# Optimization experiments

Measured on AMD Instinct MI355X. Metric: run time of the kernel, lower is better.

## Reference

```python
import jax, jax.numpy as jnp
import numpy as np

WIDE = 15
PAD = (WIDE - 1) // 2
FREQS = np.array([1., 2., 3., 4., 5., 6.], dtype=np.float32)  # wave_base_ml frequencies


def _lstm_dir(x, wih, whh, b):
    # x: [B,T,F]; wih: [4H,F]; whh: [4H,H]; b: [4H] (b_ih+b_hh fused)
    H = whh.shape[1]
    xg = jnp.einsum('btf,gf->btg', x, wih) + b  # precompute input projections
    def step(carry, xt):
        h, c = carry
        g = xt + h @ whh.T
        i, f, gg, o = jnp.split(g, 4, axis=-1)  # torch gate order i,f,g,o
        c = jax.nn.sigmoid(f) * c + jax.nn.sigmoid(i) * jnp.tanh(gg)
        h = jax.nn.sigmoid(o) * jnp.tanh(c)
        return (h, c), h
    h0 = jnp.zeros((x.shape[0], H), x.dtype)
    _, hs = jax.lax.scan(step, (h0, h0), jnp.swapaxes(xg, 0, 1))
    return jnp.swapaxes(hs, 0, 1)


def _bn(x, g, b, eps=1e-5):
    # training-mode BatchNorm1d over (N, L) per channel; x: [B,C,L]
    m = jnp.mean(x, axis=(0, 2), keepdims=True)
    v = jnp.var(x, axis=(0, 2), keepdims=True)
    return (x - m) * jax.lax.rsqrt(v + eps) * g[None, :, None] + b[None, :, None]


def _conv1d(x, w, b):
    y = jax.lax.conv_general_dilated(x, w, (1,), 'VALID', dimension_numbers=('NCH', 'OIH', 'NCH'))
    return y + b[None, :, None]


def _haar(x):
    s = 0.7071067811865476
    return (x[..., ::2] + x[..., 1::2]) * s, (x[..., ::2] - x[..., 1::2]) * s


def _forward(x, lstm_wif, lstm_whf, lstm_bf, lstm_wir, lstm_whr, lstm_br, base_w, base_b,
             g1, be1, g2, be2, g3, be3, g4, be4, g5, be5,
             w2, b2, w3, b3, w4, b4, w5, b5, fcw, fcb):
    xt = jnp.swapaxes(x, 1, 2)  # [B,T,F]
    fwd = _lstm_dir(xt, lstm_wif, lstm_whf, lstm_bf)
    bwd = _lstm_dir(xt[:, ::-1], lstm_wir, lstm_whr, lstm_br)[:, ::-1]
    X = jnp.swapaxes(jnp.concatenate([fwd, bwd], axis=-1), 1, 2)  # [B,C,T], C=2*dim
    B, C, T = X.shape
    Xp = jnp.pad(X, ((0, 0), (0, 0), (PAD, PAD)))
    # shared sliding windows [B,C,T,WIDE] used both for scale conv and Furi_conv
    Xwin = jnp.stack([Xp[..., k:k + T] for k in range(WIDE)], axis=-1)
    offs = (jnp.arange(WIDE, dtype=X.dtype) - PAD) / WIDE
    outs = []
    for ii in range(len(FREQS)):
        scales = jax.nn.relu(jnp.einsum('bctk,k->bct', Xwin, base_w[ii]) + base_b[ii])
        # per-position cosine Fourier basis generated from the learned scales
        bases = jnp.cos((2.0 * np.pi * FREQS[ii]) * scales[..., None] * offs)  # [B,C,T,WIDE]
        o = jnp.sum(Xwin * bases, axis=-1)  # position-dependent (dynamic) conv
        sqrs = jnp.sqrt((jnp.trunc(scales * WIDE) + 1.0) / (WIDE + 2) * 2.0)
        outs.append(o / sqrs)
    wave = jnp.stack(outs, axis=1).reshape(B, -1, T)  # [B, n_waves*C, T] (wave-major, matches torch cat+view)
    out = _bn(wave, g1, be1)
    out = _bn(jax.nn.relu(_conv1d(out, w2, b2)), g2, be2)
    out = _bn(jax.nn.relu(_conv1d(out, w3, b3)), g3, be3)
    out_back = out  # [B, V_dim, L3]
    out = _bn(jax.nn.relu(_conv1d(out, w4, b4)), g4, be4)  # [B,16,L3-2]
    # 4-level Haar DWT; 5 subbands upsampled to L3, averaged over channels
    a1, d1 = _haar(out_back); a2, d2 = _haar(a1); a3, d3 = _haar(a2); a4, d4 = _haar(a3)
    L3 = out_back.shape[-1]
    bands = [jnp.repeat(bb, L3 // bb.shape[-1], axis=-1) for bb in (a4, d4, d3, d2, d1)]
    dwt = jnp.stack([bb.mean(axis=1) for bb in bands], axis=1)  # [B,5,L3]
    odwt = _bn(jax.nn.relu(_conv1d(dwt, w5, b5)), g5, be5)  # [B,16,L3-2]
    out = jnp.concatenate([out, odwt], axis=-1)
    out = out.mean(axis=-1)  # AdaptiveAvgPool1d(1) + squeeze
    return out @ fcw.T + fcb


def setup_inputs() -> dict:
    key = jax.random.key(0)
    ks = iter(jax.random.split(key, 40))
    def p(shape, s=0.05):
        return jax.random.normal(next(ks), shape, jnp.float32) * s
    B, F, T, DIM, NW, Vd = 32, 64, 518, 64, 6, 32
    C = 2 * DIM
    return {
        'x': jax.random.normal(next(ks), (B, F, T), jnp.float32),
        'lstm_wif': p((4 * DIM, F)), 'lstm_whf': p((4 * DIM, DIM)), 'lstm_bf': p((4 * DIM,)),
        'lstm_wir': p((4 * DIM, F)), 'lstm_whr': p((4 * DIM, DIM)), 'lstm_br': p((4 * DIM,)),
        'base_w': p((NW, WIDE)), 'base_b': p((NW,)),
        'g1': jnp.ones((C * NW,)), 'be1': jnp.zeros((C * NW,)),
        'g2': jnp.ones((128,)), 'be2': jnp.zeros((128,)),
        'g3': jnp.ones((Vd,)), 'be3': jnp.zeros((Vd,)),
        'g4': jnp.ones((16,)), 'be4': jnp.zeros((16,)),
        'g5': jnp.ones((16,)), 'be5': jnp.zeros((16,)),
        'w2': p((128, C * NW, 3)), 'b2': p((128,)),
        'w3': p((Vd, 128, 5)), 'b3': p((Vd,)),
        'w4': p((16, Vd, 3)), 'b4': p((16,)),
        'w5': p((16, 5, 3)), 'b5': p((16,)),
        'fcw': p((10, 16)), 'fcb': p((10,)),
    }


def reference(x, lstm_wif, lstm_whf, lstm_bf, lstm_wir, lstm_whr, lstm_br, base_w, base_b,
              g1, be1, g2, be2, g3, be3, g4, be4, g5, be5,
              w2, b2, w3, b3, w4, b4, w5, b5, fcw, fcb):
    return _forward(x, lstm_wif, lstm_whf, lstm_bf, lstm_wir, lstm_whr, lstm_br, base_w, base_b,
                    g1, be1, g2, be2, g3, be3, g4, be4, g5, be5,
                    w2, b2, w3, b3, w4, b4, w5, b5, fcw, fcb)
```

## Files before the change

### kernel.cpp

```cpp
#include <hip/hip_runtime.h>
#include <math.h>

#define B_     32
#define F_     64
#define T_     518
#define HID    64
#define GATES  256
#define CCH    128
#define NWAVE  6
#define WCH    768
#define L2_    516
#define L3_    512
#define L4_    510

__device__ __forceinline__ float frcp(float x) { return __builtin_amdgcn_rcpf(x); }
__device__ __forceinline__ float fsigmoid(float x) { return frcp(1.f + __expf(-x)); }
__device__ __forceinline__ float ftanh(float x) { return 1.f - 2.f * frcp(1.f + __expf(2.f * x)); }

__global__ void xg_kernel(const float* __restrict__ x,
                          const float* __restrict__ wif, const float* __restrict__ bf,
                          const float* __restrict__ wir, const float* __restrict__ br,
                          float* __restrict__ xg_f, float* __restrict__ xg_r,
                          float* __restrict__ stats) {
    if (blockIdx.x == 0 && blockIdx.y == 0) {
        for (int i = threadIdx.x; i < 2 * WCH; i += 256) stats[i] = 0.f;
    }
    const int tid = threadIdx.x;
    const int wv  = tid >> 7;
    const int g2  = tid & 1;
    const int r   = (tid >> 1) & 63;
    const int g   = (2 * wv + g2) * 64 + r;
    const int b   = blockIdx.y;
    const int t0  = blockIdx.x * 8;
    float4 wa[16], wb[16];
    const float4* w0 = (const float4*)(wif + g * F_);
    const float4* w1 = (const float4*)(wir + g * F_);
#pragma unroll
    for (int i = 0; i < 16; ++i) { wa[i] = w0[i]; wb[i] = w1[i]; }
    const float bfv = bf[g], brv = br[g];
    for (int tt = 0; tt < 8; ++tt) {
        const int t = t0 + tt;
        if (t >= T_) break;
        const float* xp = x + (size_t)b * F_ * T_ + t;
        float a0 = bfv, a1 = brv;
#pragma unroll
        for (int i = 0; i < 16; ++i) {
            float x0 = xp[(i * 4 + 0) * T_];
            float x1 = xp[(i * 4 + 1) * T_];
            float x2 = xp[(i * 4 + 2) * T_];
            float x3 = xp[(i * 4 + 3) * T_];
            a0 += wa[i].x * x0 + wa[i].y * x1 + wa[i].z * x2 + wa[i].w * x3;
            a1 += wb[i].x * x0 + wb[i].y * x1 + wb[i].z * x2 + wb[i].w * x3;
        }
        const size_t o = ((size_t)b * T_ + t) * GATES + tid;
        xg_f[o] = a0;
        xg_r[o] = a1;
    }
}

__global__ __launch_bounds__(128, 1) void lstm_kernel(
        const float* __restrict__ xgi_f, const float* __restrict__ xgi_r,
        const float* __restrict__ whf, const float* __restrict__ whr,
        float* __restrict__ X) {
    const int dir = blockIdx.x & 1;
    const int b   = blockIdx.x >> 1;
    const float* xg  = (dir ? xgi_r : xgi_f) + (size_t)b * T_ * GATES;
    const float* whh = dir ? whr : whf;
    const int tid = threadIdx.x;
    const int r   = tid & 63;
    const int w   = tid >> 6;

    float4 wA[16], wB[16];
    {
        const float4* pA = (const float4*)(whh + (size_t)((2 * w) * HID + r) * HID);
        const float4* pB = (const float4*)(whh + (size_t)((2 * w + 1) * HID + r) * HID);
#pragma unroll
        for (int i = 0; i < 16; ++i) { wA[i] = pA[i]; wB[i] = pB[i]; }
    }

    __shared__ __align__(16) float hs[2][HID];
    __shared__ __align__(16) float gbuf[2][HID][4];
    hs[w][r] = 0.f;
    float c = 0.f;
    float* Xrow = X + ((size_t)(b * CCH + dir * HID + r)) * T_;

    int t = dir ? (T_ - 1) : 0;
    const int step = dir ? -1 : 1;
    const float2* xg2 = (const float2*)xg;
    float2 q0 = xg2[((size_t)t * 2 + w) * 64 + r];
    float2 q1 = xg2[((size_t)(t + step) * 2 + w) * 64 + r];

    for (int s = 0; s < T_; ++s) {
        float4 a0 = {q0.x, 0.f, 0.f, 0.f};
        float4 a1 = {q0.y, 0.f, 0.f, 0.f};
        const float4* h4p = (const float4*)hs[w];
#pragma unroll
        for (int i = 0; i < 16; ++i) {
            const float4 h4 = h4p[i];
            a0.x = fmaf(wA[i].x, h4.x, a0.x); a0.y = fmaf(wA[i].y, h4.y, a0.y);
            a0.z = fmaf(wA[i].z, h4.z, a0.z); a0.w = fmaf(wA[i].w, h4.w, a0.w);
            a1.x = fmaf(wB[i].x, h4.x, a1.x); a1.y = fmaf(wB[i].y, h4.y, a1.y);
            a1.z = fmaf(wB[i].z, h4.z, a1.z); a1.w = fmaf(wB[i].w, h4.w, a1.w);
        }
        const float gA = (a0.x + a0.y) + (a0.z + a0.w);
        const float gB = (a1.x + a1.y) + (a1.z + a1.w);
        const int buf = s & 1;
        *(float2*)&gbuf[buf][r][2 * w] = make_float2(gA, gB);

        int tp = t + 2 * step;
        tp = tp < 0 ? 0 : (tp >= T_ ? T_ - 1 : tp);
        const float2 qn = xg2[((size_t)tp * 2 + w) * 64 + r];

        asm volatile("s_waitcnt lgkmcnt(0)" ::: "memory");
        __builtin_amdgcn_s_barrier();

        const float4 g4 = *(const float4*)gbuf[buf][r];
        const float si = fsigmoid(g4.x);
        const float sf = fsigmoid(g4.y);
        const float so = fsigmoid(g4.w);
        c = sf * c + si * ftanh(g4.z);
        const float h = so * ftanh(c);

        hs[w][r] = h;
        if (w == 0) Xrow[t] = h;
        q0 = q1; q1 = qn;
        t += step;
    }
}

__global__ void wave_kernel(const float* __restrict__ X,
                            const float* __restrict__ bw, const float* __restrict__ bb,
                            float* __restrict__ wave, float* __restrict__ stats) {
    const int b = blockIdx.z, c = blockIdx.y;
    const int t0 = blockIdx.x * 256;
    const int tid = threadIdx.x;
    __shared__ float xs[256 + 14];
    __shared__ float bws[NWAVE][16];
    __shared__ float bbs[NWAVE];
    __shared__ float red[4][12];
    const float* xrow = X + ((size_t)(b * CCH + c)) * T_;
    for (int i = tid; i < 270; i += 256) {
        int tt = t0 - 7 + i;
        xs[i] = (tt >= 0 && tt < T_) ? xrow[tt] : 0.f;
    }
    if (tid < NWAVE * 15) bws[tid / 15][tid % 15] = bw[tid];
    if (tid < NWAVE) bbs[tid] = bb[tid];
    __syncthreads();
    const int t = t0 + tid;
    float ls[NWAVE], lq[NWAVE];
#pragma unroll
    for (int ii = 0; ii < NWAVE; ++ii) { ls[ii] = 0.f; lq[ii] = 0.f; }
    if (t < T_) {
        float win[15];
#pragma unroll
        for (int k = 0; k < 15; ++k) win[k] = xs[tid + k];
        float e[8];
        e[0] = win[7];
#pragma unroll
        for (int m = 1; m < 8; ++m) e[m] = win[7 - m] + win[7 + m];
        const float c0 = 6.28318530717958647692f / 15.f;
#pragma unroll
        for (int ii = 0; ii < NWAVE; ++ii) {
            float sc = bbs[ii];
#pragma unroll
            for (int k = 0; k < 15; ++k) sc += win[k] * bws[ii][k];
            sc = fmaxf(sc, 0.f);
            const float phi = c0 * (float)(ii + 1) * sc;
            float o = e[0];
#pragma unroll
            for (int m = 1; m < 8; ++m) o += e[m] * __cosf(phi * (float)m);
            const float q = (truncf(sc * 15.f) + 1.f) * (2.f / 17.f);
            const float val = o * rsqrtf(q);
            wave[((size_t)(b * WCH + ii * CCH + c)) * T_ + t] = val;
            ls[ii] = val;
            lq[ii] = val * val;
        }
    }
#pragma unroll
    for (int off = 32; off > 0; off >>= 1) {
#pragma unroll
        for (int ii = 0; ii < NWAVE; ++ii) {
            ls[ii] += __shfl_down(ls[ii], off);
            lq[ii] += __shfl_down(lq[ii], off);
        }
    }
    if ((tid & 63) == 0) {
        const int w = tid >> 6;
#pragma unroll
        for (int ii = 0; ii < NWAVE; ++ii) { red[w][ii] = ls[ii]; red[w][6 + ii] = lq[ii]; }
    }
    __syncthreads();
    if (tid < 12) {
        const float a = red[0][tid] + red[1][tid] + red[2][tid] + red[3][tid];
        const int ii = tid % 6;
        const int ch = ii * CCH + c;
        atomicAdd(&stats[(tid >= 6 ? WCH : 0) + ch], a);
    }
}

__global__ void bn1_finalize_kernel(const float* __restrict__ stats,
                                    float* __restrict__ mean, float* __restrict__ rstd) {
    const int c = threadIdx.x;
    const float n = (float)(B_ * T_);
    const float m = stats[c] / n;
    const float v = stats[WCH + c] / n - m * m;
    mean[c] = m;
    rstd[c] = rsqrtf(v + 1e-5f);
}

__global__ void bn_stats_kernel(const float* __restrict__ x, int Bn, int C, int L,
                                float* __restrict__ mean, float* __restrict__ rstd) {
    const int c = blockIdx.x;
    const int tid = threadIdx.x;
    float s = 0.f, s2 = 0.f;
    for (int b = 0; b < Bn; ++b) {
        const float* row = x + ((size_t)b * C + c) * L;
        for (int l = tid; l < L; l += 256) { float v = row[l]; s += v; s2 += v * v; }
    }
#pragma unroll
    for (int off = 32; off > 0; off >>= 1) { s += __shfl_down(s, off); s2 += __shfl_down(s2, off); }
    __shared__ float ss[4], ss2[4];
    if ((tid & 63) == 0) { ss[tid >> 6] = s; ss2[tid >> 6] = s2; }
    __syncthreads();
    if (tid == 0) {
        float S = ss[0] + ss[1] + ss[2] + ss[3];
        float S2 = ss2[0] + ss2[1] + ss2[2] + ss2[3];
        float n = (float)(Bn * L);
        float m = S / n;
        float v = S2 / n - m * m;
        mean[c] = m;
        rstd[c] = rsqrtf(v + 1e-5f);
    }
}

__global__ void bnfold2_kernel(const float* __restrict__ w2, const float* __restrict__ b2,
                               const float* __restrict__ m1, const float* __restrict__ r1,
                               const float* __restrict__ g1, const float* __restrict__ be1,
                               float* __restrict__ w2t, float* __restrict__ b2t) {
    const int o = blockIdx.x, tid = threadIdx.x;
    float part = 0.f;
    for (int idx = tid; idx < WCH * 3; idx += 256) {
        const int c = idx / 3;
        const float sc = r1[c] * g1[c];
        const float sh = be1[c] - m1[c] * sc;
        const float wv = w2[(size_t)o * (WCH * 3) + idx];
        w2t[(size_t)idx * 128 + o] = wv * sc;
        part += wv * sh;
    }
#pragma unroll
    for (int off = 32; off > 0; off >>= 1) part += __shfl_down(part, off);
    __shared__ float red[4];
    if ((tid & 63) == 0) red[tid >> 6] = part;
    __syncthreads();
    if (tid == 0) b2t[o] = b2[o] + red[0] + red[1] + red[2] + red[3];
}

__global__ void bnfold3_kernel(const float* __restrict__ w3, const float* __restrict__ b3,
                               const float* __restrict__ m2, const float* __restrict__ r2,
                               const float* __restrict__ g2, const float* __restrict__ be2,
                               float* __restrict__ w3t, float* __restrict__ b3t) {
    const int o = blockIdx.x, tid = threadIdx.x;
    float part = 0.f;
    for (int idx = tid; idx < 128 * 5; idx += 256) {
        const int c = idx / 5;
        const float sc = r2[c] * g2[c];
        const float sh = be2[c] - m2[c] * sc;
        const float wv = w3[(size_t)o * 640 + idx];
        w3t[(size_t)idx * 32 + o] = wv * sc;
        part += wv * sh;
    }
#pragma unroll
    for (int off = 32; off > 0; off >>= 1) part += __shfl_down(part, off);
    __shared__ float red[4];
    if ((tid & 63) == 0) red[tid >> 6] = part;
    __syncthreads();
    if (tid == 0) b3t[o] = b3[o] + red[0] + red[1] + red[2] + red[3];
}

__global__ void bnfold4_kernel(const float* __restrict__ w4, const float* __restrict__ b4,
                               const float* __restrict__ m3, const float* __restrict__ r3,
                               const float* __restrict__ g3, const float* __restrict__ be3,
                               float* __restrict__ w4t, float* __restrict__ b4t,
                               float* __restrict__ bnp3) {
    const int o = blockIdx.x, tid = threadIdx.x;
    float part = 0.f;
    if (tid < 96) {
        const int c = tid / 3;
        const float sc = r3[c] * g3[c];
        const float sh = be3[c] - m3[c] * sc;
        const float wv = w4[(size_t)o * 96 + tid];
        w4t[(size_t)tid * 16 + o] = wv * sc;
        part = wv * sh;
    }
    if (o == 0 && tid >= 96) {
        const int ch = tid - 96;
        const float sc = r3[ch] * g3[ch];
        bnp3[ch] = sc;
        bnp3[32 + ch] = be3[ch] - m3[ch] * sc;
    }
#pragma unroll
    for (int off = 32; off > 0; off >>= 1) part += __shfl_down(part, off);
    __shared__ float red[2];
    if ((tid & 63) == 0) red[tid >> 6] = part;
    __syncthreads();
    if (tid == 0) b4t[o] = b4[o] + red[0] + red[1];
}

__global__ __launch_bounds__(256) void conv2_kernel(
        const float* __restrict__ in, const float* __restrict__ wt,
        const float* __restrict__ bt, float* __restrict__ out) {
    const int b  = blockIdx.x;
    const int t  = blockIdx.y * 256 + threadIdx.x;
    const int o0 = blockIdx.z * 16;
    if (t >= L2_) return;
    float acc[16];
#pragma unroll
    for (int j = 0; j < 16; ++j) acc[j] = bt[o0 + j];
    const float* inb = in + (size_t)b * WCH * T_ + t;
    for (int c = 0; c < WCH; ++c) {
        const float x0 = inb[c * T_], x1 = inb[c * T_ + 1], x2 = inb[c * T_ + 2];
        const float* wc = wt + (size_t)c * 384 + o0;
#pragma unroll
        for (int j = 0; j < 16; ++j)
            acc[j] = fmaf(x0, wc[j], fmaf(x1, wc[128 + j], fmaf(x2, wc[256 + j], acc[j])));
    }
    const size_t ob = ((size_t)b * 128 + o0) * L2_ + t;
#pragma unroll
    for (int j = 0; j < 16; ++j) out[ob + (size_t)j * L2_] = fmaxf(acc[j], 0.f);
}

__global__ __launch_bounds__(256) void conv3_kernel(
        const float* __restrict__ in, const float* __restrict__ wt,
        const float* __restrict__ bt, float* __restrict__ out) {
    const int b  = blockIdx.x;
    const int t  = blockIdx.y * 256 + threadIdx.x;
    const int o0 = blockIdx.z * 8;
    float acc[8];
#pragma unroll
    for (int j = 0; j < 8; ++j) acc[j] = bt[o0 + j];
    const float* inb = in + (size_t)b * 128 * L2_ + t;
    for (int c = 0; c < 128; ++c) {
        const float x0 = inb[c * L2_], x1 = inb[c * L2_ + 1], x2 = inb[c * L2_ + 2];
        const float x3 = inb[c * L2_ + 3], x4 = inb[c * L2_ + 4];
        const float* wc = wt + (size_t)c * 160 + o0;
#pragma unroll
        for (int j = 0; j < 8; ++j) {
            float a = fmaf(x0, wc[j], acc[j]);
            a = fmaf(x1, wc[32 + j], a);
            a = fmaf(x2, wc[64 + j], a);
            a = fmaf(x3, wc[96 + j], a);
            acc[j] = fmaf(x4, wc[128 + j], a);
        }
    }
    const size_t ob = ((size_t)b * 32 + o0) * L3_ + t;
#pragma unroll
    for (int j = 0; j < 8; ++j) out[ob + (size_t)j * L3_] = fmaxf(acc[j], 0.f);
}

__global__ __launch_bounds__(256) void conv4_kernel(
        const float* __restrict__ in, const float* __restrict__ wt,
        const float* __restrict__ bt, float* __restrict__ out) {
    const int b = blockIdx.x;
    const int t = blockIdx.y * 256 + threadIdx.x;
    if (t >= L4_) return;
    float acc[16];
#pragma unroll
    for (int j = 0; j < 16; ++j) acc[j] = bt[j];
    const float* inb = in + (size_t)b * 32 * L3_ + t;
    for (int c = 0; c < 32; ++c) {
        const float x0 = inb[c * L3_], x1 = inb[c * L3_ + 1], x2 = inb[c * L3_ + 2];
        const float* wc = wt + (size_t)c * 48;
#pragma unroll
        for (int j = 0; j < 16; ++j)
            acc[j] = fmaf(x0, wc[j], fmaf(x1, wc[16 + j], fmaf(x2, wc[32 + j], acc[j])));
    }
    const size_t ob = ((size_t)b * 16) * L4_ + t;
#pragma unroll
    for (int j = 0; j < 16; ++j) out[ob + (size_t)j * L4_] = fmaxf(acc[j], 0.f);
}

__global__ __launch_bounds__(512) void dwt_conv5_kernel(const float* __restrict__ y3,
                                                        const float* __restrict__ w5,
                                                        const float* __restrict__ b5,
                                                        const float* __restrict__ bnp3,
                                                        float* __restrict__ y5) {
    const int b = blockIdx.x, l = threadIdx.x;
    __shared__ float cm[L3_];
    __shared__ float bands[5][L3_];
    __shared__ float w5s[240];
    __shared__ float b5s[16];
    __shared__ float sc3s[32], sh3s[32];
    if (l < 240) w5s[l] = w5[l];
    if (l < 16) b5s[l] = b5[l];
    if (l >= 256 && l < 288) sc3s[l - 256] = bnp3[l - 256];
    if (l >= 288 && l < 320) sh3s[l - 288] = bnp3[32 + (l - 288)];
    __syncthreads();
    float s = 0.f, shs = 0.f;
    for (int ch = 0; ch < 32; ++ch) {
        s = fmaf(y3[((size_t)b * 32 + ch) * L3_ + l], sc3s[ch], s);
        shs += sh3s[ch];
    }
    cm[l] = (s + shs) * (1.f / 32.f);
    __syncthreads();
    const float s1 = 0.70710678118654752440f;
    const float s2c = 0.5f;
    const float s3 = 0.35355339059327378f;
    const float s4 = 0.25f;
    const int b16 = l & ~15, b8 = l & ~7, b4v = l & ~3, b2v = l & ~1;
    float sa = 0.f, sb = 0.f;
#pragma unroll
    for (int i = 0; i < 8; ++i) { sa += cm[b16 + i]; sb += cm[b16 + 8 + i]; }
    bands[0][l] = (sa + sb) * s4;
    bands[1][l] = (sa - sb) * s4;
    float ta = 0.f, tb = 0.f;
#pragma unroll
    for (int i = 0; i < 4; ++i) { ta += cm[b8 + i]; tb += cm[b8 + 4 + i]; }
    bands[2][l] = (ta - tb) * s3;
    bands[3][l] = (cm[b4v] + cm[b4v + 1] - cm[b4v + 2] - cm[b4v + 3]) * s2c;
    bands[4][l] = (cm[b2v] - cm[b2v + 1]) * s1;
    __syncthreads();
    if (l < L4_) {
        float in3[5][3];
#pragma unroll
        for (int c = 0; c < 5; ++c) {
            in3[c][0] = bands[c][l]; in3[c][1] = bands[c][l + 1]; in3[c][2] = bands[c][l + 2];
        }
#pragma unroll
        for (int o = 0; o < 16; ++o) {
            float acc = b5s[o];
#pragma unroll
            for (int c = 0; c < 5; ++c) {
                const float* wp = &w5s[(o * 5 + c) * 3];
                acc += in3[c][0] * wp[0] + in3[c][1] * wp[1] + in3[c][2] * wp[2];
            }
            y5[((size_t)b * 16 + o) * L4_ + l] = fmaxf(acc, 0.f);
        }
    }
}

__global__ __launch_bounds__(512) void tail_final_kernel(
        const float* __restrict__ y4, const float* __restrict__ y5,
        const float* __restrict__ g4, const float* __restrict__ be4,
        const float* __restrict__ g5, const float* __restrict__ be5,
        const float* __restrict__ fcw, const float* __restrict__ fcb,
        float* __restrict__ out) {
    const int p = threadIdx.x;
    const int b = p >> 4, ch = p & 15;
    const float2* p4 = (const float2*)(y4 + ((size_t)(b * 16 + ch)) * L4_);
    const float2* p5 = (const float2*)(y5 + ((size_t)(b * 16 + ch)) * L4_);
    float s4 = 0.f, q4 = 0.f, s5 = 0.f, q5 = 0.f;
    for (int i = 0; i < L4_ / 2; ++i) {
        float2 a = p4[i], bb2 = p5[i];
        s4 += a.x + a.y;  q4 += a.x * a.x + a.y * a.y;
        s5 += bb2.x + bb2.y; q5 += bb2.x * bb2.x + bb2.y * bb2.y;
    }
    __shared__ float S4[512], Q4[512], S5[512], Q5[512];
    __shared__ float M4[16], R4[16], M5[16], R5[16];
    __shared__ float pool[B_][16];
    S4[p] = s4; Q4[p] = q4; S5[p] = s5; Q5[p] = q5;
    __syncthreads();
    if (p < 16) {
        float ts = 0.f, tq = 0.f, us = 0.f, uq = 0.f;
        for (int bb = 0; bb < B_; ++bb) {
            ts += S4[bb * 16 + p]; tq += Q4[bb * 16 + p];
            us += S5[bb * 16 + p]; uq += Q5[bb * 16 + p];
        }
        const float n = (float)(B_ * L4_);
        float m = ts / n; M4[p] = m; R4[p] = rsqrtf(tq / n - m * m + 1e-5f);
        m = us / n;       M5[p] = m; R5[p] = rsqrtf(uq / n - m * m + 1e-5f);
    }
    __syncthreads();
    {
        const float mm4 = s4 / (float)L4_, mm5 = s5 / (float)L4_;
        const float v4 = (mm4 - M4[ch]) * R4[ch] * g4[ch] + be4[ch];
        const float v5 = (mm5 - M5[ch]) * R5[ch] * g5[ch] + be5[ch];
        pool[b][ch] = 0.5f * (v4 + v5);
    }
    __syncthreads();
    if (p < B_ * 10) {
        const int bb = p / 10, row = p - bb * 10;
        float a = fcb[row];
#pragma unroll
        for (int c = 0; c < 16; ++c) a += pool[bb][c] * fcw[row * 16 + c];
        out[bb * 10 + row] = a;
    }
}

extern "C" void kernel_launch(void* const* d_in, const int* in_sizes, int n_in,
                              void* d_out, int out_size, void* d_ws, size_t ws_size,
                              hipStream_t stream) {
    (void)in_sizes; (void)n_in; (void)out_size; (void)ws_size;
    const float* x   = (const float*)d_in[0];
    const float* wif = (const float*)d_in[1];
    const float* whf = (const float*)d_in[2];
    const float* bf  = (const float*)d_in[3];
    const float* wir = (const float*)d_in[4];
    const float* whr = (const float*)d_in[5];
    const float* br  = (const float*)d_in[6];
    const float* bw  = (const float*)d_in[7];
    const float* bb  = (const float*)d_in[8];
    const float* g1  = (const float*)d_in[9];  const float* be1 = (const float*)d_in[10];
    const float* g2  = (const float*)d_in[11]; const float* be2 = (const float*)d_in[12];
    const float* g3  = (const float*)d_in[13]; const float* be3 = (const float*)d_in[14];
    const float* g4  = (const float*)d_in[15]; const float* be4 = (const float*)d_in[16];
    const float* g5  = (const float*)d_in[17]; const float* be5 = (const float*)d_in[18];
    const float* w2  = (const float*)d_in[19]; const float* b2  = (const float*)d_in[20];
    const float* w3  = (const float*)d_in[21]; const float* b3  = (const float*)d_in[22];
    const float* w4  = (const float*)d_in[23]; const float* b4  = (const float*)d_in[24];
    const float* w5  = (const float*)d_in[25]; const float* b5  = (const float*)d_in[26];
    const float* fcw = (const float*)d_in[27]; const float* fcb = (const float*)d_in[28];
    float* out = (float*)d_out;
    float* ws  = (float*)d_ws;

    float* xg_f  = ws;
    float* xg_r  = ws + 4243456;
    float* wave  = ws;
    float* X     = ws + 12730368;
    float* y2    = ws + 14852096;
    float* y3    = ws + 16965632;
    float* y4    = ws + 17489920;
    float* y5    = ws + 17751040;
    float* stats = ws + 18012160;
    float* m1 = ws + 18013696; float* r1 = m1 + 768;
    float* m2 = r1 + 768;      float* r2 = m2 + 128;
    float* m3 = r2 + 128;      float* r3 = m3 + 32;
    float* w2t  = X;
    float* b2t  = X + 294912;
    float* w3t  = X + 295040;
    float* b3t  = X + 315520;
    float* w4t  = X + 315552;
    float* b4t  = X + 317088;
    float* bnp3 = X + 317104;

    xg_kernel<<<dim3(65, 32), 256, 0, stream>>>(x, wif, bf, wir, br, xg_f, xg_r, stats);
    lstm_kernel<<<dim3(64), 128, 0, stream>>>(xg_f, xg_r, whf, whr, X);
    wave_kernel<<<dim3(3, CCH, B_), 256, 0, stream>>>(X, bw, bb, wave, stats);
    bn1_finalize_kernel<<<dim3(1), 768, 0, stream>>>(stats, m1, r1);
    bnfold2_kernel<<<dim3(128), 256, 0, stream>>>(w2, b2, m1, r1, g1, be1, w2t, b2t);
    conv2_kernel<<<dim3(32, 3, 8), 256, 0, stream>>>(wave, w2t, b2t, y2);
    bn_stats_kernel<<<dim3(128), 256, 0, stream>>>(y2, B_, 128, L2_, m2, r2);
    bnfold3_kernel<<<dim3(32), 256, 0, stream>>>(w3, b3, m2, r2, g2, be2, w3t, b3t);
    conv3_kernel<<<dim3(32, 2, 4), 256, 0, stream>>>(y2, w3t, b3t, y3);
    bn_stats_kernel<<<dim3(32), 256, 0, stream>>>(y3, B_, 32, L3_, m3, r3);
    bnfold4_kernel<<<dim3(16), 128, 0, stream>>>(w4, b4, m3, r3, g3, be3, w4t, b4t, bnp3);
    conv4_kernel<<<dim3(32, 2), 256, 0, stream>>>(y3, w4t, b4t, y4);
    dwt_conv5_kernel<<<dim3(B_), 512, 0, stream>>>(y3, w5, b5, bnp3, y5);
    tail_final_kernel<<<dim3(1), 512, 0, stream>>>(y4, y5, g4, be4, g5, be5, fcw, fcb, out);
}
```

Before: 1.022 ms.

## Split LSTM gate rows across four waves with one gate per thread

The recurrent LSTM kernel now runs 256 threads per block, so each wave computes one gate type and each thread holds a single 64-wide weight row, where before each thread held two rows. This halves the per-thread dot-product chain on the serial critical path and uses half the weight registers. The xg layout changes to natural gate order, and the prefetch of input projections is deepened to four steps. In exchange, each step's barrier now spans four waves, and every thread stores the hidden state into a per-wave copy of the shared buffer.

```diff
diff --git a/kernel.cpp b/kernel.cpp
--- a/kernel.cpp
+++ b/kernel.cpp
@@ -26,10 +26,7 @@
         for (int i = threadIdx.x; i < 2 * WCH; i += 256) stats[i] = 0.f;
     }
     const int tid = threadIdx.x;
-    const int wv  = tid >> 7;
-    const int g2  = tid & 1;
-    const int r   = (tid >> 1) & 63;
-    const int g   = (2 * wv + g2) * 64 + r;
+    const int g   = tid;
     const int b   = blockIdx.y;
     const int t0  = blockIdx.x * 8;
     float4 wa[16], wb[16];
@@ -58,7 +55,7 @@
     }
 }
 
-__global__ __launch_bounds__(128, 1) void lstm_kernel(
+__global__ __launch_bounds__(256, 1) void lstm_kernel(
         const float* __restrict__ xgi_f, const float* __restrict__ xgi_r,
         const float* __restrict__ whf, const float* __restrict__ whr,
         float* __restrict__ X) {
@@ -70,60 +67,67 @@
     const int r   = tid & 63;
     const int w   = tid >> 6;
 
-    float4 wA[16], wB[16];
+    float4 wv[16];
     {
-        const float4* pA = (const float4*)(whh + (size_t)((2 * w) * HID + r) * HID);
-        const float4* pB = (const float4*)(whh + (size_t)((2 * w + 1) * HID + r) * HID);
-#pragma unroll
-        for (int i = 0; i < 16; ++i) { wA[i] = pA[i]; wB[i] = pB[i]; }
-    }
-
-    __shared__ __align__(16) float hs[2][HID];
-    __shared__ __align__(16) float gbuf[2][HID][4];
+        const float4* pW = (const float4*)(whh + (size_t)(w * HID + r) * HID);
+#pragma unroll
+        for (int i = 0; i < 16; ++i) wv[i] = pW[i];
+    }
+
+    __shared__ __align__(16) float hs[4][HID];
+    __shared__ __align__(16) float gbuf[2][4][HID];
     hs[w][r] = 0.f;
     float c = 0.f;
     float* Xrow = X + ((size_t)(b * CCH + dir * HID + r)) * T_;
 
     int t = dir ? (T_ - 1) : 0;
     const int step = dir ? -1 : 1;
-    const float2* xg2 = (const float2*)xg;
-    float2 q0 = xg2[((size_t)t * 2 + w) * 64 + r];
-    float2 q1 = xg2[((size_t)(t + step) * 2 + w) * 64 + r];
+    const int gidx = w * HID + r;
+
+    int tp;
+    tp = t;                                      float q0 = xg[(size_t)tp * GATES + gidx];
+    tp = t + step;     tp = tp < 0 ? 0 : (tp >= T_ ? T_ - 1 : tp);
+    float q1 = xg[(size_t)tp * GATES + gidx];
+    tp = t + 2 * step; tp = tp < 0 ? 0 : (tp >= T_ ? T_ - 1 : tp);
+    float q2 = xg[(size_t)tp * GATES + gidx];
+    tp = t + 3 * step; tp = tp < 0 ? 0 : (tp >= T_ ? T_ - 1 : tp);
+    float q3 = xg[(size_t)tp * GATES + gidx];
 
     for (int s = 0; s < T_; ++s) {
-        float4 a0 = {q0.x, 0.f, 0.f, 0.f};
-        float4 a1 = {q0.y, 0.f, 0.f, 0.f};
+        float4 acc = {q0, 0.f, 0.f, 0.f};
         const float4* h4p = (const float4*)hs[w];
 #pragma unroll
         for (int i = 0; i < 16; ++i) {
             const float4 h4 = h4p[i];
-            a0.x = fmaf(wA[i].x, h4.x, a0.x); a0.y = fmaf(wA[i].y, h4.y, a0.y);
-            a0.z = fmaf(wA[i].z, h4.z, a0.z); a0.w = fmaf(wA[i].w, h4.w, a0.w);
-            a1.x = fmaf(wB[i].x, h4.x, a1.x); a1.y = fmaf(wB[i].y, h4.y, a1.y);
-            a1.z = fmaf(wB[i].z, h4.z, a1.z); a1.w = fmaf(wB[i].w, h4.w, a1.w);
-        }
-        const float gA = (a0.x + a0.y) + (a0.z + a0.w);
-        const float gB = (a1.x + a1.y) + (a1.z + a1.w);
+            acc.x = fmaf(wv[i].x, h4.x, acc.x);
+            acc.y = fmaf(wv[i].y, h4.y, acc.y);
+            acc.z = fmaf(wv[i].z, h4.z, acc.z);
+            acc.w = fmaf(wv[i].w, h4.w, acc.w);
+        }
+        const float ga = (acc.x + acc.y) + (acc.z + acc.w);
         const int buf = s & 1;
-        *(float2*)&gbuf[buf][r][2 * w] = make_float2(gA, gB);
-
-        int tp = t + 2 * step;
+        gbuf[buf][w][r] = ga;
+
+        tp = t + 4 * step;
         tp = tp < 0 ? 0 : (tp >= T_ ? T_ - 1 : tp);
-        const float2 qn = xg2[((size_t)tp * 2 + w) * 64 + r];
+        const float qn = xg[(size_t)tp * GATES + gidx];
 
         asm volatile("s_waitcnt lgkmcnt(0)" ::: "memory");
         __builtin_amdgcn_s_barrier();
 
-        const float4 g4 = *(const float4*)gbuf[buf][r];
-        const float si = fsigmoid(g4.x);
-        const float sf = fsigmoid(g4.y);
-        const float so = fsigmoid(g4.w);
-        c = sf * c + si * ftanh(g4.z);
+        const float gi = gbuf[buf][0][r];
+        const float gf = gbuf[buf][1][r];
+        const float gg = gbuf[buf][2][r];
+        const float go = gbuf[buf][3][r];
+        const float si = fsigmoid(gi);
+        const float sf = fsigmoid(gf);
+        const float so = fsigmoid(go);
+        c = sf * c + si * ftanh(gg);
         const float h = so * ftanh(c);
 
         hs[w][r] = h;
         if (w == 0) Xrow[t] = h;
-        q0 = q1; q1 = qn;
+        q0 = q1; q1 = q2; q2 = q3; q3 = qn;
         t += step;
     }
 }
@@ -533,7 +537,7 @@
     float* bnp3 = X + 317104;
 
     xg_kernel<<<dim3(65, 32), 256, 0, stream>>>(x, wif, bf, wir, br, xg_f, xg_r, stats);
-    lstm_kernel<<<dim3(64), 128, 0, stream>>>(xg_f, xg_r, whf, whr, X);
+    lstm_kernel<<<dim3(64), 256, 0, stream>>>(xg_f, xg_r, whf, whr, X);
     wave_kernel<<<dim3(3, CCH, B_), 256, 0, stream>>>(X, bw, bb, wave, stats);
     bn1_finalize_kernel<<<dim3(1), 768, 0, stream>>>(stats, m1, r1);
     bnfold2_kernel<<<dim3(128), 256, 0, stream>>>(w2, b2, m1, r1, g1, be1, w2t, b2t);
```

Measured after the change: 1.092 ms. 1.07x slower.
